# Kernel tuning notes

Measured on AMD Instinct MI355X. Metric: run time of the kernel, lower is better.

## Reference

```python
import jax, jax.numpy as jnp
import numpy as np

B, D, K = 16384, 32, 128  # batch, cluster_dim, num_clusters


def setup_inputs() -> dict:
    key = jax.random.key(0)
    x = jax.random.normal(key, (B, D, K), dtype=jnp.float32)
    mu_0 = jnp.zeros((D, K), dtype=jnp.float32)                      # running mean buffer
    L_0 = jnp.broadcast_to(jnp.eye(D, dtype=jnp.float32), (K, D, D)) # running Cholesky buffer
    n_0 = jnp.ones((1,), dtype=jnp.float32)                          # running count
    return {"x": x, "mu_0": mu_0, "L_0": L_0, "n_0": n_0}


def reference(x, mu_0, L_0, n_0):
    # Training-mode forward of ClusterNorm1dv2.
    Bn = x.shape[0]
    eps_eye = jnp.eye(x.shape[1], dtype=x.dtype)
    n0 = n_0[0]
    x_mu = jnp.mean(x, axis=0)                         # [D, K]
    x_cnt = jnp.transpose(x - x_mu[None], (2, 1, 0))   # [K, D, B]
    C = jnp.einsum('kdb,keb->kde', x_cnt, x_cnt)       # [K, D, D] per-cluster scatter
    denom = n0 + Bn
    new_mu = (n0 * mu_0 + Bn * x_mu) / denom           # [D, K]
    x_d = jnp.transpose((x_mu - mu_0)[None], (2, 1, 0))  # [K, D, 1]
    new_cov = (jnp.einsum('kde,kfe->kdf', L_0, L_0) * (n0 / denom)
               + C / denom
               + jnp.einsum('kdo,keo->kde', x_d, x_d) * (n0 * Bn / denom ** 2))
    L = jnp.linalg.cholesky(new_cov + eps_eye)         # [K, D, D]
    xc = jnp.transpose(x - new_mu[None], (2, 1, 0))    # [K, D, B]
    Z = jax.scipy.linalg.solve_triangular(L, xc, lower=True)  # whitening solve
    return jnp.transpose(Z, (2, 1, 0))                 # [B, D, K]
```

## Files before the change

kernel.cpp:

```cpp
#include <hip/hip_runtime.h>

typedef __attribute__((ext_vector_type(4))) float f32x4;

#define NB 16384
#define ND 32
#define NK 128

template<int SP>
__device__ __forceinline__ void k1_body(const float* __restrict__ x,
                                        float* __restrict__ part,
                                        float* __restrict__ vs,
                                        int k0, int b0, int t) {
  constexpr int CL = 4*(SP+1);
  constexpr int CH = 4*(8-SP);
  const int sd = t >> 3, sj = t & 7;
  const int kl = t & 63;

  float aL[4][CL];
  float aH[4][CH];
  float ssum[8];
  #pragma unroll
  for (int r=0;r<4;r++){
    #pragma unroll
    for (int c=0;c<CL;c++) aL[r][c]=0.f;
    #pragma unroll
    for (int c=0;c<CH;c++) aH[r][c]=0.f;
  }
  #pragma unroll
  for (int i=0;i<8;i++) ssum[i]=0.f;

  const float* src0 = x + ((size_t)b0*ND + sd)*NK + k0 + 4*sj;

  f32x4 rc[2][2], rn[2][2];
  #pragma unroll
  for (int s=0;s<2;s++){
    const float* src = src0 + (size_t)s*4096;
    rc[s][0] = *(const f32x4*)src;
    rc[s][1] = *(const f32x4*)(src+32);
  }

  for (int g=0; g<32; ++g) {
    if (g < 31) {
      #pragma unroll
      for (int s=0;s<2;s++){
        const float* src = src0 + (size_t)(2*(g+1)+s)*4096;
        rn[s][0] = *(const f32x4*)src;
        rn[s][1] = *(const f32x4*)(src+32);
      }
    }
    float* dstbuf = vs + (g&1)*4608;
    #pragma unroll
    for (int s=0;s<2;s++){
      float* dst = dstbuf + s*2304;
      #pragma unroll
      for (int i=0;i<4;i++){
        dst[(4*sj+i)*36 + sd]    = rc[s][0][i];
        dst[(4*sj+32+i)*36 + sd] = rc[s][1][i];
        ssum[i]   += rc[s][0][i];
        ssum[4+i] += rc[s][1][i];
      }
    }
    __syncthreads();
    #pragma unroll
    for (int s=0;s<2;s++){
      const float* row = dstbuf + s*2304 + kl*36;
      f32x4 bv[8-SP];
      #pragma unroll
      for (int q=0;q<8-SP;q++) bv[q] = *(const f32x4*)(row + 4*q);
      #pragma unroll
      for (int r=0;r<4;r++){
        const float al = bv[SP][r];
        const float ah = bv[7-SP][r];
        #pragma unroll
        for (int q=0;q<=SP;q++){
          #pragma unroll
          for (int i=0;i<4;i++) aL[r][4*q+i] += al*bv[q][i];
        }
        #pragma unroll
        for (int q=0;q<8-SP;q++){
          #pragma unroll
          for (int i=0;i<4;i++) aH[r][4*q+i] += ah*bv[q][i];
        }
      }
    }
    #pragma unroll
    for (int s=0;s<2;s++){ rc[s][0]=rn[s][0]; rc[s][1]=rn[s][1]; }
  }

  float* pb = part + (size_t)blockIdx.x*38912;
  #pragma unroll
  for (int r=0;r<4;r++){
    #pragma unroll
    for (int c=0;c<CL;c++)
      __builtin_nontemporal_store(aL[r][c], &pb[(8*SP*(SP+1) + r*CL + c)*64 + kl]);
    #pragma unroll
    for (int c=0;c<CH;c++)
      __builtin_nontemporal_store(aH[r][c], &pb[(8*(7-SP)*(8-SP) + r*CH + c)*64 + kl]);
  }
  #pragma unroll
  for (int i=0;i<4;i++){
    __builtin_nontemporal_store(ssum[i],   &pb[(576+sd)*64 + 4*sj + i]);
    __builtin_nontemporal_store(ssum[4+i], &pb[(576+sd)*64 + 32 + 4*sj + i]);
  }
}

__global__ __launch_bounds__(256, 2) void k1_scatter(const float* __restrict__ x,
                                                     float* __restrict__ part) {
  __shared__ float vs[2*4608];
  const int t = threadIdx.x;
  const int ktile = blockIdx.x & 1;
  const int chunk = blockIdx.x >> 1;
  const int k0 = ktile*64, b0 = chunk*64;
  switch (t>>6) {
    case 0:  k1_body<0>(x, part, vs, k0, b0, t); break;
    case 1:  k1_body<1>(x, part, vs, k0, b0, t); break;
    case 2:  k1_body<2>(x, part, vs, k0, b0, t); break;
    default: k1_body<3>(x, part, vs, k0, b0, t); break;
  }
}

__global__ void k2a_reduce(const float* __restrict__ part, float* __restrict__ sfin) {
  const int t = threadIdx.x;
  const int bx = blockIdx.x;
  const int h = bx & 1, ktile = (bx>>1)&1, vg = bx>>2;
  const int vidx = vg*4 + (t>>6);
  const int kl = t & 63;
  const float* p = part + ((size_t)(h*128)*2 + ktile)*38912 + vidx*64 + kl;
  float a0=0.f,a1=0.f,a2=0.f,a3=0.f;
  for (int c=0;c<128;c+=4){
    a0 += __builtin_nontemporal_load(&p[(size_t)(c+0)*77824]);
    a1 += __builtin_nontemporal_load(&p[(size_t)(c+1)*77824]);
    a2 += __builtin_nontemporal_load(&p[(size_t)(c+2)*77824]);
    a3 += __builtin_nontemporal_load(&p[(size_t)(c+3)*77824]);
  }
  sfin[h*77824 + vidx*128 + ktile*64 + kl] = (a0+a1)+(a2+a3);
}

__global__ void k2b_chol(const float* __restrict__ sfin,
                         const float* __restrict__ mu0,
                         const float* __restrict__ L0,
                         const float* __restrict__ n0p,
                         float* __restrict__ lpad,
                         float* __restrict__ nmu) {
  const int k = blockIdx.x;
  const int t = threadIdx.x;
  __shared__ float L0s[32*33];
  __shared__ float Am[32*33];
  __shared__ float xdl[32];
  __shared__ float dinv[32];
  const float n0 = n0p[0];
  const float denom = n0 + (float)NB;

  for (int idx = t; idx < 1024; idx += 256)
    L0s[(idx>>5)*33 + (idx&31)] = L0[k*1024 + idx];
  if (t < 32) {
    const float S  = sfin[(576+t)*128 + k] + sfin[77824 + (576+t)*128 + k];
    const float m0 = mu0[t*128 + k];
    nmu[t*128 + k] = (n0*m0 + S) / denom;
    xdl[t] = S*(1.0f/NB) - m0;
  }
  __syncthreads();

  const float c1 = n0/denom, c2 = 1.0f/denom;
  const float c3 = n0*(float)NB/(denom*denom);
  for (int idx = t; idx < 1024; idx += 256) {
    const int d = idx>>5, e = idx&31;
    const int dd = d>=e?d:e, ee = d>=e?e:d;
    const int R = dd>>2;
    const int vi = 8*R*(R+1) + (dd&3)*4*(R+1) + ee;
    const float M  = sfin[vi*128 + k]      + sfin[77824 + vi*128 + k];
    const float Sd = sfin[(576+d)*128 + k] + sfin[77824 + (576+d)*128 + k];
    const float Se = sfin[(576+e)*128 + k] + sfin[77824 + (576+e)*128 + k];
    const float C = M - Sd*Se*(1.0f/NB);
    float g = 0.f;
    #pragma unroll 8
    for (int f=0; f<32; f++) g += L0s[d*33+f]*L0s[e*33+f];
    float a = g*c1 + C*c2 + xdl[d]*xdl[e]*c3;
    if (d==e) a += 1.0f;
    Am[d*33+e] = a;
  }
  __syncthreads();

  for (int j=0;j<32;j++){
    float acc = 0.f;
    if (t < 32 && t >= j) {
      acc = Am[t*33+j];
      for (int e=0;e<j;e++) acc -= Am[t*33+e]*Am[j*33+e];
    }
    __syncthreads();
    if (t == j) {
      const float dj = sqrtf(acc);
      Am[j*33+j] = dj;
      dinv[j] = 1.0f/dj;
    }
    __syncthreads();
    if (t < 32 && t > j) Am[t*33+j] = acc*dinv[j];
    __syncthreads();
  }

  if (t < 32) {
    const int d = t;
    int rs = 0;
    for (int e=0;e<d;e++) rs += (e+3)>>2;
    rs *= 4;
    const int rl = ((d+3)>>2)*4;
    float* lp = lpad + k*576;
    for (int e=0;e<rl;e++) lp[rs+e] = (e<d) ? Am[d*33+e] : 0.f;
    lp[544+d] = dinv[d];
  }
}

__global__ __launch_bounds__(256, 2) void k3_whiten(const float* __restrict__ x,
                                                    const float* __restrict__ lpad,
                                                    const float* __restrict__ nmu,
                                                    float* __restrict__ out) {
  __shared__ float Lw[32*580];
  __shared__ float muL[32*32];
  const int t = threadIdx.x;
  const int bx = blockIdx.x;
  const int m = (bx >> 3) & 1;
  const int u = ((bx >> 4) << 3) | (bx & 7);
  const int ktile = ((u & 1) << 1) | m;
  const int chunk = u >> 1;
  const int k0 = ktile*32;

  {
    const f32x4* src = (const f32x4*)(lpad + (size_t)k0*576);
    #pragma unroll
    for (int q=0;q<18;q++){
      const int idx = t + q*256;
      const int row = idx/144, col = idx - row*144;
      *(f32x4*)(&Lw[row*580 + col*4]) = src[idx];
    }
    #pragma unroll
    for (int idx=t; idx<1024; idx+=256)
      muL[idx] = nmu[(idx>>5)*128 + k0 + (idx&31)];
  }
  __syncthreads();

  const int kl = t & 31;
  const int so = t >> 5;
  const float* Lrow = &Lw[kl*580];
  const int b0 = chunk*128;

  for (int it=0; it<4; ++it) {
    const int base = b0 + it*32 + so;
    const float* xa = x + (size_t)(base     )*4096 + k0 + kl;
    const float* xb = x + (size_t)(base +  8)*4096 + k0 + kl;
    const float* xc = x + (size_t)(base + 16)*4096 + k0 + kl;
    const float* xd = x + (size_t)(base + 24)*4096 + k0 + kl;
    float vA[32], vB[32], vC[32], vD[32];
    #pragma unroll
    for (int d=0; d<32; ++d) vA[d] = xa[d*128];
    #pragma unroll
    for (int d=0; d<32; ++d) vB[d] = xb[d*128];
    #pragma unroll
    for (int d=0; d<32; ++d) vC[d] = xc[d*128];
    #pragma unroll
    for (int d=0; d<32; ++d) vD[d] = xd[d*128];
    #pragma unroll
    for (int d=0; d<32; ++d) {
      const float m2 = muL[d*32 + kl];
      vA[d] -= m2; vB[d] -= m2; vC[d] -= m2; vD[d] -= m2;
    }
    int rs = 0;
    #pragma unroll
    for (int d=0; d<32; ++d) {
      float sA = vA[d], sB = vB[d], sC = vC[d], sD = vD[d];
      const int nq = (d+3)>>2;
      #pragma unroll
      for (int q=0; q<nq; ++q) {
        const f32x4 Lq = *(const f32x4*)(Lrow + rs + 4*q);
        sA -= Lq[0]*vA[4*q+0] + Lq[1]*vA[4*q+1] + Lq[2]*vA[4*q+2] + Lq[3]*vA[4*q+3];
        sB -= Lq[0]*vB[4*q+0] + Lq[1]*vB[4*q+1] + Lq[2]*vB[4*q+2] + Lq[3]*vB[4*q+3];
        sC -= Lq[0]*vC[4*q+0] + Lq[1]*vC[4*q+1] + Lq[2]*vC[4*q+2] + Lq[3]*vC[4*q+3];
        sD -= Lq[0]*vD[4*q+0] + Lq[1]*vD[4*q+1] + Lq[2]*vD[4*q+2] + Lq[3]*vD[4*q+3];
      }
      const float di = Lrow[544+d];
      vA[d] = sA*di; vB[d] = sB*di; vC[d] = sC*di; vD[d] = sD*di;
      rs += 4*nq;
    }
    float* oa = out + (size_t)(base     )*4096 + k0 + kl;
    float* ob = out + (size_t)(base +  8)*4096 + k0 + kl;
    float* oc = out + (size_t)(base + 16)*4096 + k0 + kl;
    float* od = out + (size_t)(base + 24)*4096 + k0 + kl;
    #pragma unroll
    for (int d=0; d<32; ++d) __builtin_nontemporal_store(vA[d], oa + d*128);
    #pragma unroll
    for (int d=0; d<32; ++d) __builtin_nontemporal_store(vB[d], ob + d*128);
    #pragma unroll
    for (int d=0; d<32; ++d) __builtin_nontemporal_store(vC[d], oc + d*128);
    #pragma unroll
    for (int d=0; d<32; ++d) __builtin_nontemporal_store(vD[d], od + d*128);
  }
}

extern "C" void kernel_launch(void* const* d_in, const int* in_sizes, int n_in,
                              void* d_out, int out_size, void* d_ws, size_t ws_size,
                              hipStream_t stream) {
  const float* x   = (const float*)d_in[0];
  const float* mu0 = (const float*)d_in[1];
  const float* L0  = (const float*)d_in[2];
  const float* n0  = (const float*)d_in[3];
  float* out  = (float*)d_out;
  float* part = out;
  float* sfin = out + 20971520;
  float* lpad = (float*)d_ws;
  float* nmu  = lpad + 128*576;

  k1_scatter<<<512, 256, 0, stream>>>(x, part);
  k2a_reduce<<<608, 256, 0, stream>>>(part, sfin);
  k2b_chol  <<<128, 256, 0, stream>>>(sfin, mu0, L0, n0, lpad, nmu);
  k3_whiten <<<512, 256, 0, stream>>>(x, lpad, nmu, out);
}
```

Before: 227.8 us.

## Load scatter inputs directly from global memory, dropping LDS staging and barriers

The scatter kernel no longer stages x tiles through shared memory with a double buffer and __syncthreads. Each wavefront now reads its own column slice of x straight from global memory, coalesced across the 64 k lanes, with scalar loads per d. Per-wave column sums are written only for the rows each wave owns. This removes LDS traffic and block-wide barriers. In exchange, each wave re-reads overlapping rows from global memory or cache, loses the explicit register prefetch, and issues many scalar loads.

```diff
diff --git a/kernel.cpp b/kernel.cpp
--- a/kernel.cpp
+++ b/kernel.cpp
@@ -9,12 +9,10 @@
 template<int SP>
 __device__ __forceinline__ void k1_body(const float* __restrict__ x,
                                         float* __restrict__ part,
-                                        float* __restrict__ vs,
-                                        int k0, int b0, int t) {
+                                        int k0, int b0, int kl) {
   constexpr int CL = 4*(SP+1);
   constexpr int CH = 4*(8-SP);
-  const int sd = t >> 3, sj = t & 7;
-  const int kl = t & 63;
+  constexpr int NV = CH;
 
   float aL[4][CL];
   float aH[4][CH];
@@ -29,62 +27,24 @@
   #pragma unroll
   for (int i=0;i<8;i++) ssum[i]=0.f;
 
-  const float* src0 = x + ((size_t)b0*ND + sd)*NK + k0 + 4*sj;
-
-  f32x4 rc[2][2], rn[2][2];
-  #pragma unroll
-  for (int s=0;s<2;s++){
-    const float* src = src0 + (size_t)s*4096;
-    rc[s][0] = *(const f32x4*)src;
-    rc[s][1] = *(const f32x4*)(src+32);
-  }
-
-  for (int g=0; g<32; ++g) {
-    if (g < 31) {
+  const float* xp = x + (size_t)b0*4096 + k0 + kl;
+
+  for (int s=0; s<64; ++s) {
+    const float* xs = xp + (size_t)s*4096;
+    float v[NV];
+    #pragma unroll
+    for (int d=0; d<NV; ++d) v[d] = xs[d*128];
+    #pragma unroll
+    for (int r=0;r<4;r++){ ssum[r] += v[4*SP+r]; ssum[4+r] += v[CH-4+r]; }
+    #pragma unroll
+    for (int r=0;r<4;r++){
+      const float al = v[4*SP+r];
       #pragma unroll
-      for (int s=0;s<2;s++){
-        const float* src = src0 + (size_t)(2*(g+1)+s)*4096;
-        rn[s][0] = *(const f32x4*)src;
-        rn[s][1] = *(const f32x4*)(src+32);
-      }
-    }
-    float* dstbuf = vs + (g&1)*4608;
-    #pragma unroll
-    for (int s=0;s<2;s++){
-      float* dst = dstbuf + s*2304;
+      for (int c=0;c<CL;c++) aL[r][c] += al*v[c];
+      const float ah = v[CH-4+r];
       #pragma unroll
-      for (int i=0;i<4;i++){
-        dst[(4*sj+i)*36 + sd]    = rc[s][0][i];
-        dst[(4*sj+32+i)*36 + sd] = rc[s][1][i];
-        ssum[i]   += rc[s][0][i];
-        ssum[4+i] += rc[s][1][i];
-      }
-    }
-    __syncthreads();
-    #pragma unroll
-    for (int s=0;s<2;s++){
-      const float* row = dstbuf + s*2304 + kl*36;
-      f32x4 bv[8-SP];
-      #pragma unroll
-      for (int q=0;q<8-SP;q++) bv[q] = *(const f32x4*)(row + 4*q);
-      #pragma unroll
-      for (int r=0;r<4;r++){
-        const float al = bv[SP][r];
-        const float ah = bv[7-SP][r];
-        #pragma unroll
-        for (int q=0;q<=SP;q++){
-          #pragma unroll
-          for (int i=0;i<4;i++) aL[r][4*q+i] += al*bv[q][i];
-        }
-        #pragma unroll
-        for (int q=0;q<8-SP;q++){
-          #pragma unroll
-          for (int i=0;i<4;i++) aH[r][4*q+i] += ah*bv[q][i];
-        }
-      }
-    }
-    #pragma unroll
-    for (int s=0;s<2;s++){ rc[s][0]=rn[s][0]; rc[s][1]=rn[s][1]; }
+      for (int c=0;c<CH;c++) aH[r][c] += ah*v[c];
+    }
   }
 
   float* pb = part + (size_t)blockIdx.x*38912;
@@ -98,24 +58,24 @@
       __builtin_nontemporal_store(aH[r][c], &pb[(8*(7-SP)*(8-SP) + r*CH + c)*64 + kl]);
   }
   #pragma unroll
-  for (int i=0;i<4;i++){
-    __builtin_nontemporal_store(ssum[i],   &pb[(576+sd)*64 + 4*sj + i]);
-    __builtin_nontemporal_store(ssum[4+i], &pb[(576+sd)*64 + 32 + 4*sj + i]);
+  for (int r=0;r<4;r++){
+    __builtin_nontemporal_store(ssum[r],   &pb[(576 + 4*SP + r)*64 + kl]);
+    __builtin_nontemporal_store(ssum[4+r], &pb[(576 + CH-4 + r)*64 + kl]);
   }
 }
 
 __global__ __launch_bounds__(256, 2) void k1_scatter(const float* __restrict__ x,
                                                      float* __restrict__ part) {
-  __shared__ float vs[2*4608];
   const int t = threadIdx.x;
   const int ktile = blockIdx.x & 1;
   const int chunk = blockIdx.x >> 1;
   const int k0 = ktile*64, b0 = chunk*64;
+  const int kl = t & 63;
   switch (t>>6) {
-    case 0:  k1_body<0>(x, part, vs, k0, b0, t); break;
-    case 1:  k1_body<1>(x, part, vs, k0, b0, t); break;
-    case 2:  k1_body<2>(x, part, vs, k0, b0, t); break;
-    default: k1_body<3>(x, part, vs, k0, b0, t); break;
+    case 0:  k1_body<0>(x, part, k0, b0, kl); break;
+    case 1:  k1_body<1>(x, part, k0, b0, kl); break;
+    case 2:  k1_body<2>(x, part, k0, b0, kl); break;
+    default: k1_body<3>(x, part, k0, b0, kl); break;
   }
 }
 
```

Result: faster. 200.5 us (-12.0%).
